# Optimization experiments

Measured on AMD Instinct MI355X. Metric: run time of the kernel, lower is better.

Reference implementation:

```python
import jax, jax.numpy as jnp
import numpy as np

N_EMBD = 4096
N_LAYERS = 32
LAYER = 3


def _layer_norm(x, w, b, eps=1e-5):
    mu = jnp.mean(x)
    var = jnp.var(x)
    return (x - mu) * jax.lax.rsqrt(var + eps) * w + b


def setup_inputs() -> dict:
    key = jax.random.key(0)
    ks = jax.random.split(key, 12)
    s = np.float32(1.0 / np.sqrt(N_EMBD))  # keep matvec outputs O(1) so exp() stays sane
    return {
        "input": jax.random.normal(ks[0], (N_EMBD,), jnp.float32),
        "state": jax.random.normal(ks[1], (5 * N_LAYERS, N_EMBD), jnp.float32) * 0.1,
        "time_mix_k": jax.random.uniform(ks[2], (N_EMBD,), jnp.float32),
        "time_mix_v": jax.random.uniform(ks[3], (N_EMBD,), jnp.float32),
        "time_mix_r": jax.random.uniform(ks[4], (N_EMBD,), jnp.float32),
        "time_first": jax.random.normal(ks[5], (N_EMBD,), jnp.float32) * 0.5,
        "time_decay": -jnp.abs(jax.random.normal(ks[6], (N_EMBD,), jnp.float32)),
        "kw": jax.random.normal(ks[7], (N_EMBD, N_EMBD), jnp.float32) * s,
        "vw": jax.random.normal(ks[8], (N_EMBD, N_EMBD), jnp.float32) * s,
        "rw": jax.random.normal(ks[9], (N_EMBD, N_EMBD), jnp.float32) * s,
        "ow": jax.random.normal(ks[10], (N_EMBD, N_EMBD), jnp.float32) * s,
        "ln_weight": jnp.ones((N_EMBD,), jnp.float32),
        "ln_bias": jnp.zeros((N_EMBD,), jnp.float32),
        "layer_num": LAYER,
        "n_embd": N_EMBD,
    }


def reference(input, state, time_mix_k, time_mix_v, time_mix_r, time_first,
              time_decay, kw, vw, rw, ow, ln_weight, ln_bias, layer_num, n_embd):
    # FLOAT_MODE == 'fp32' branch of the original module.
    i = int(layer_num)
    x = _layer_norm(input, ln_weight, ln_bias)

    prev = state[5 * i + 1]  # previous token's post-LN x (time shift)
    xk = x * time_mix_k + prev * (1.0 - time_mix_k)
    xv = x * time_mix_v + prev * (1.0 - time_mix_v)
    xr = x * time_mix_r + prev * (1.0 - time_mix_r)

    r = jax.nn.sigmoid(rw @ xr)
    kk = kw @ xk
    vv = vw @ xv

    aa = state[5 * i + 2]
    bb = state[5 * i + 3]
    pp = state[5 * i + 4]  # running log-max for numerical stability

    # WKV output for this token
    ww = time_first + kk
    p = jnp.maximum(pp, ww)
    e1 = jnp.exp(pp - p)
    e2 = jnp.exp(ww - p)
    a = e1 * aa + e2 * vv
    b = e1 * bb + e2

    # state update
    ww2 = pp + time_decay
    p2 = jnp.maximum(ww2, kk)
    e1s = jnp.exp(ww2 - p2)
    e2s = jnp.exp(kk - p2)
    new_aa = e1s * aa + e2s * vv
    new_bb = e1s * bb + e2s

    new_state = (state
                 .at[5 * i + 1].set(x)
                 .at[5 * i + 2].set(new_aa)
                 .at[5 * i + 3].set(new_bb)
                 .at[5 * i + 4].set(p2))

    wkv = a / b
    out = ow @ (r * wkv)
    return (new_state, out)
```

## Files before the change

### kernel.cpp

```cpp
#include <hip/hip_runtime.h>
#include <math.h>

#define NE 4096
#define NROWS_STATE 160

#define WS_XK   0
#define WS_XV   (NE)
#define WS_XR   (2*NE)
#define WS_KK   (3*NE)
#define WS_VV   (4*NE)
#define WS_RR   (5*NE)
#define WS_RWKV (6*NE)

__device__ __forceinline__ float wave_reduce_sum(float v) {
    #pragma unroll
    for (int off = 32; off > 0; off >>= 1)
        v += __shfl_down(v, off, 64);
    return v;
}

__global__ void __launch_bounds__(256)
k_copy_ln_mix(const float* __restrict__ in, const float* __restrict__ state,
              const float* __restrict__ tmk, const float* __restrict__ tmv,
              const float* __restrict__ tmr, const float* __restrict__ lnw,
              const float* __restrict__ lnb, const int* __restrict__ layer,
              float* __restrict__ out_state, float* __restrict__ out_vec,
              float* __restrict__ ws) {
    int li = layer[0];
    if (blockIdx.x >= 641) {
        int zidx = (blockIdx.x - 641) * 256 + threadIdx.x;
        float4 z = make_float4(0.f, 0.f, 0.f, 0.f);
        if (zidx < 3 * NE / 4) ((float4*)(ws + WS_KK))[zidx] = z;
        else                   ((float4*)out_vec)[zidx - 3 * NE / 4] = z;
        return;
    }
    if (blockIdx.x != 0) {
        int i4 = (blockIdx.x - 1) * 256 + threadIdx.x;
        int row = i4 >> 10;
        if (row < 5 * li + 1 || row > 5 * li + 4) {
            ((float4*)out_state)[i4] = ((const float4*)state)[i4];
        }
        return;
    }
    __shared__ float sm1[4];
    __shared__ float sm2[4];
    __shared__ float s_mu, s_rstd;
    int t = threadIdx.x;
    int lane = t & 63, wid = t >> 6;

    float4 v[4];
    float sum = 0.0f, sumsq = 0.0f;
    #pragma unroll
    for (int j = 0; j < 4; ++j) {
        v[j] = ((const float4*)in)[t * 4 + j];
        sum   += v[j].x + v[j].y + v[j].z + v[j].w;
        sumsq += v[j].x*v[j].x + v[j].y*v[j].y + v[j].z*v[j].z + v[j].w*v[j].w;
    }
    float s1 = wave_reduce_sum(sum);
    float s2 = wave_reduce_sum(sumsq);
    if (lane == 0) { sm1[wid] = s1; sm2[wid] = s2; }
    __syncthreads();
    if (t == 0) {
        float tot  = sm1[0] + sm1[1] + sm1[2] + sm1[3];
        float tot2 = sm2[0] + sm2[1] + sm2[2] + sm2[3];
        float mu  = tot * (1.0f / NE);
        float var = tot2 * (1.0f / NE) - mu * mu;
        s_mu = mu;
        s_rstd = rsqrtf(var + 1e-5f);
    }
    __syncthreads();
    float mu = s_mu, rstd = s_rstd;

    const float* prev_row = state + (size_t)(5 * li + 1) * NE;
    float* x_row = out_state + (size_t)(5 * li + 1) * NE;

    #pragma unroll
    for (int j = 0; j < 4; ++j) {
        #pragma unroll
        for (int c = 0; c < 4; ++c) {
            int idx = t * 16 + j * 4 + c;
            float xin = (c == 0) ? v[j].x : (c == 1) ? v[j].y : (c == 2) ? v[j].z : v[j].w;
            float x    = (xin - mu) * rstd * lnw[idx] + lnb[idx];
            float prev = prev_row[idx];
            float mk = tmk[idx], mv = tmv[idx], mr = tmr[idx];
            ws[WS_XK + idx] = x * mk + prev * (1.0f - mk);
            ws[WS_XV + idx] = x * mv + prev * (1.0f - mv);
            ws[WS_XR + idx] = x * mr + prev * (1.0f - mr);
            x_row[idx] = x;
        }
    }
}

__global__ void __launch_bounds__(256)
k_matvec3(const float* __restrict__ kw, const float* __restrict__ vw,
          const float* __restrict__ rw, const float* __restrict__ ws_in,
          float* __restrict__ ws_out) {
    int t    = threadIdx.x;
    int lane = t & 63;
    int g    = blockIdx.x * 4 + (t >> 6);
    int m    = g >> 14;
    int rem  = g & 16383;
    int row  = rem >> 2;
    int seg  = rem & 3;
    const float* W = (m == 0) ? kw : (m == 1) ? vw : rw;
    const float4* Wr = (const float4*)(W + (size_t)row * NE) + seg * 256;
    const float4* xv = (const float4*)(ws_in + m * NE) + seg * 256;

    float acc = 0.0f;
    #pragma unroll
    for (int i = 0; i < 4; ++i) {
        float4 w4 = Wr[i * 64 + lane];
        float4 x4 = xv[i * 64 + lane];
        acc += w4.x*x4.x + w4.y*x4.y + w4.z*x4.z + w4.w*x4.w;
    }
    acc = wave_reduce_sum(acc);
    if (lane == 0) atomicAdd(&ws_out[m * NE + row], acc);
}

__global__ void k_wkv(const float* __restrict__ state, const float* __restrict__ tf,
                      const float* __restrict__ td, const int* __restrict__ layer,
                      const float* __restrict__ ws, float* __restrict__ out_state,
                      float* __restrict__ rwkv) {
    int idx = blockIdx.x * blockDim.x + threadIdx.x;
    if (idx >= NE) return;
    int li = layer[0];
    float kk = ws[WS_KK + idx];
    float vv = ws[WS_VV + idx];
    float r  = 1.0f / (1.0f + expf(-ws[WS_RR + idx]));
    float aa = state[(size_t)(5 * li + 2) * NE + idx];
    float bb = state[(size_t)(5 * li + 3) * NE + idx];
    float pp = state[(size_t)(5 * li + 4) * NE + idx];

    float ww = tf[idx] + kk;
    float p  = fmaxf(pp, ww);
    float e1 = expf(pp - p);
    float e2 = expf(ww - p);
    float a  = e1 * aa + e2 * vv;
    float b  = e1 * bb + e2;

    float ww2 = pp + td[idx];
    float p2  = fmaxf(ww2, kk);
    float e1s = expf(ww2 - p2);
    float e2s = expf(kk - p2);
    out_state[(size_t)(5 * li + 2) * NE + idx] = e1s * aa + e2s * vv;
    out_state[(size_t)(5 * li + 3) * NE + idx] = e1s * bb + e2s;
    out_state[(size_t)(5 * li + 4) * NE + idx] = p2;

    rwkv[idx] = r * (a / b);
}

__global__ void __launch_bounds__(256)
k_matvec_ow(const float* __restrict__ ow, const float* __restrict__ rwkv,
            float* __restrict__ out) {
    int t    = threadIdx.x;
    int lane = t & 63;
    int g    = blockIdx.x * 4 + (t >> 6);
    int row  = g >> 2;
    int seg  = g & 3;
    const float4* Wr = (const float4*)(ow + (size_t)row * NE) + seg * 256;
    const float4* xv = (const float4*)rwkv + seg * 256;

    float acc = 0.0f;
    #pragma unroll
    for (int i = 0; i < 4; ++i) {
        float4 w4 = Wr[i * 64 + lane];
        float4 x4 = xv[i * 64 + lane];
        acc += w4.x*x4.x + w4.y*x4.y + w4.z*x4.z + w4.w*x4.w;
    }
    acc = wave_reduce_sum(acc);
    if (lane == 0) atomicAdd(&out[row], acc);
}

extern "C" void kernel_launch(void* const* d_in, const int* in_sizes, int n_in,
                              void* d_out, int out_size, void* d_ws, size_t ws_size,
                              hipStream_t stream) {
    const float* input = (const float*)d_in[0];
    const float* state = (const float*)d_in[1];
    const float* tmk   = (const float*)d_in[2];
    const float* tmv   = (const float*)d_in[3];
    const float* tmr   = (const float*)d_in[4];
    const float* tf    = (const float*)d_in[5];
    const float* td    = (const float*)d_in[6];
    const float* kw    = (const float*)d_in[7];
    const float* vw    = (const float*)d_in[8];
    const float* rw    = (const float*)d_in[9];
    const float* ow    = (const float*)d_in[10];
    const float* lnw   = (const float*)d_in[11];
    const float* lnb   = (const float*)d_in[12];
    const int*   layer = (const int*)d_in[13];

    float* out_state = (float*)d_out;
    float* out_vec   = (float*)d_out + (size_t)NROWS_STATE * NE;
    float* ws        = (float*)d_ws;

    k_copy_ln_mix<<<657, 256, 0, stream>>>(input, state, tmk, tmv, tmr, lnw, lnb,
                                           layer, out_state, out_vec, ws);
    k_matvec3<<<3 * NE, 256, 0, stream>>>(kw, vw, rw, ws, ws + WS_KK);
    k_wkv<<<NE / 256, 256, 0, stream>>>(state, tf, td, layer, ws, out_state,
                                        ws + WS_RWKV);
    k_matvec_ow<<<NE, 256, 0, stream>>>(ow, ws + WS_RWKV, out_vec);
}
```

Baseline: 56.48 us.

## Fuse layernorm and mixing into k/v/r matvec, drop atomics and zeroing

Every block of the k/v/r matvec kernel now recomputes the layernorm statistics and the token-mix vector into shared memory, which removes the separate mix kernel and its workspace round trip. Each wave computes a full row dot product, so the split-row atomicAdds and the zero-initialisation of outputs are no longer needed. The state copy moves into the wkv kernel, and the ow matvec stages its input vector in shared memory. The cost is redundant layernorm work in roughly three thousand blocks and 16 KB of shared memory per block, which may reduce occupancy.

```diff
diff --git a/kernel.cpp b/kernel.cpp
--- a/kernel.cpp
+++ b/kernel.cpp
@@ -4,13 +4,10 @@
 #define NE 4096
 #define NROWS_STATE 160
 
-#define WS_XK   0
-#define WS_XV   (NE)
-#define WS_XR   (2*NE)
-#define WS_KK   (3*NE)
-#define WS_VV   (4*NE)
-#define WS_RR   (5*NE)
-#define WS_RWKV (6*NE)
+#define WS_KK   0
+#define WS_VV   (NE)
+#define WS_RR   (2*NE)
+#define WS_RWKV (3*NE)
 
 __device__ __forceinline__ float wave_reduce_sum(float v) {
     #pragma unroll
@@ -20,33 +17,18 @@
 }
 
 __global__ void __launch_bounds__(256)
-k_copy_ln_mix(const float* __restrict__ in, const float* __restrict__ state,
-              const float* __restrict__ tmk, const float* __restrict__ tmv,
-              const float* __restrict__ tmr, const float* __restrict__ lnw,
-              const float* __restrict__ lnb, const int* __restrict__ layer,
-              float* __restrict__ out_state, float* __restrict__ out_vec,
-              float* __restrict__ ws) {
+k_ln_matvec3(const float* __restrict__ in, const float* __restrict__ state,
+             const float* __restrict__ tmk, const float* __restrict__ tmv,
+             const float* __restrict__ tmr, const float* __restrict__ lnw,
+             const float* __restrict__ lnb, const int* __restrict__ layer,
+             const float* __restrict__ kw, const float* __restrict__ vw,
+             const float* __restrict__ rw, float* __restrict__ out_state,
+             float* __restrict__ ws_out) {
+    __shared__ float4 sx[NE / 4];
+    __shared__ float sred[8];
+    __shared__ float s_stats[2];
+    int t = threadIdx.x, lane = t & 63, wid = t >> 6;
     int li = layer[0];
-    if (blockIdx.x >= 641) {
-        int zidx = (blockIdx.x - 641) * 256 + threadIdx.x;
-        float4 z = make_float4(0.f, 0.f, 0.f, 0.f);
-        if (zidx < 3 * NE / 4) ((float4*)(ws + WS_KK))[zidx] = z;
-        else                   ((float4*)out_vec)[zidx - 3 * NE / 4] = z;
-        return;
-    }
-    if (blockIdx.x != 0) {
-        int i4 = (blockIdx.x - 1) * 256 + threadIdx.x;
-        int row = i4 >> 10;
-        if (row < 5 * li + 1 || row > 5 * li + 4) {
-            ((float4*)out_state)[i4] = ((const float4*)state)[i4];
-        }
-        return;
-    }
-    __shared__ float sm1[4];
-    __shared__ float sm2[4];
-    __shared__ float s_mu, s_rstd;
-    int t = threadIdx.x;
-    int lane = t & 63, wid = t >> 6;
 
     float4 v[4];
     float sum = 0.0f, sumsq = 0.0f;
@@ -58,72 +40,77 @@
     }
     float s1 = wave_reduce_sum(sum);
     float s2 = wave_reduce_sum(sumsq);
-    if (lane == 0) { sm1[wid] = s1; sm2[wid] = s2; }
+    if (lane == 0) { sred[wid] = s1; sred[4 + wid] = s2; }
     __syncthreads();
     if (t == 0) {
-        float tot  = sm1[0] + sm1[1] + sm1[2] + sm1[3];
-        float tot2 = sm2[0] + sm2[1] + sm2[2] + sm2[3];
+        float tot  = sred[0] + sred[1] + sred[2] + sred[3];
+        float tot2 = sred[4] + sred[5] + sred[6] + sred[7];
         float mu  = tot * (1.0f / NE);
         float var = tot2 * (1.0f / NE) - mu * mu;
-        s_mu = mu;
-        s_rstd = rsqrtf(var + 1e-5f);
+        s_stats[0] = mu;
+        s_stats[1] = rsqrtf(var + 1e-5f);
     }
     __syncthreads();
-    float mu = s_mu, rstd = s_rstd;
+    float mu = s_stats[0], rstd = s_stats[1];
 
+    if (blockIdx.x >= 3072) {
+        int e = (blockIdx.x - 3072) * 256 + t;
+        float x = (in[e] - mu) * rstd * lnw[e] + lnb[e];
+        out_state[(size_t)(5 * li + 1) * NE + e] = x;
+        return;
+    }
+
+    int m    = blockIdx.x >> 10;
+    int rowg = blockIdx.x & 1023;
+    const float* tm = (m == 0) ? tmk : (m == 1) ? tmv : tmr;
     const float* prev_row = state + (size_t)(5 * li + 1) * NE;
-    float* x_row = out_state + (size_t)(5 * li + 1) * NE;
 
     #pragma unroll
     for (int j = 0; j < 4; ++j) {
-        #pragma unroll
-        for (int c = 0; c < 4; ++c) {
-            int idx = t * 16 + j * 4 + c;
-            float xin = (c == 0) ? v[j].x : (c == 1) ? v[j].y : (c == 2) ? v[j].z : v[j].w;
-            float x    = (xin - mu) * rstd * lnw[idx] + lnb[idx];
-            float prev = prev_row[idx];
-            float mk = tmk[idx], mv = tmv[idx], mr = tmr[idx];
-            ws[WS_XK + idx] = x * mk + prev * (1.0f - mk);
-            ws[WS_XV + idx] = x * mv + prev * (1.0f - mv);
-            ws[WS_XR + idx] = x * mr + prev * (1.0f - mr);
-            x_row[idx] = x;
-        }
+        int i4 = t * 4 + j;
+        float4 xin = v[j];
+        float4 tm4 = ((const float4*)tm)[i4];
+        float4 pv4 = ((const float4*)prev_row)[i4];
+        float4 lw4 = ((const float4*)lnw)[i4];
+        float4 lb4 = ((const float4*)lnb)[i4];
+        float4 r;
+        r.x = ((xin.x - mu) * rstd * lw4.x + lb4.x) * tm4.x + pv4.x * (1.0f - tm4.x);
+        r.y = ((xin.y - mu) * rstd * lw4.y + lb4.y) * tm4.y + pv4.y * (1.0f - tm4.y);
+        r.z = ((xin.z - mu) * rstd * lw4.z + lb4.z) * tm4.z + pv4.z * (1.0f - tm4.z);
+        r.w = ((xin.w - mu) * rstd * lw4.w + lb4.w) * tm4.w + pv4.w * (1.0f - tm4.w);
+        sx[i4] = r;
     }
+    __syncthreads();
+
+    int row = rowg * 4 + wid;
+    const float* W = (m == 0) ? kw : (m == 1) ? vw : rw;
+    const float4* Wr = (const float4*)(W + (size_t)row * NE);
+    float acc = 0.0f;
+    #pragma unroll
+    for (int i = 0; i < 16; ++i) {
+        float4 w4 = Wr[i * 64 + lane];
+        float4 x4 = sx[i * 64 + lane];
+        acc += w4.x*x4.x + w4.y*x4.y + w4.z*x4.z + w4.w*x4.w;
+    }
+    acc = wave_reduce_sum(acc);
+    if (lane == 0) ws_out[m * NE + row] = acc;
 }
 
 __global__ void __launch_bounds__(256)
-k_matvec3(const float* __restrict__ kw, const float* __restrict__ vw,
-          const float* __restrict__ rw, const float* __restrict__ ws_in,
-          float* __restrict__ ws_out) {
-    int t    = threadIdx.x;
-    int lane = t & 63;
-    int g    = blockIdx.x * 4 + (t >> 6);
-    int m    = g >> 14;
-    int rem  = g & 16383;
-    int row  = rem >> 2;
-    int seg  = rem & 3;
-    const float* W = (m == 0) ? kw : (m == 1) ? vw : rw;
-    const float4* Wr = (const float4*)(W + (size_t)row * NE) + seg * 256;
-    const float4* xv = (const float4*)(ws_in + m * NE) + seg * 256;
-
-    float acc = 0.0f;
-    #pragma unroll
-    for (int i = 0; i < 4; ++i) {
-        float4 w4 = Wr[i * 64 + lane];
-        float4 x4 = xv[i * 64 + lane];
-        acc += w4.x*x4.x + w4.y*x4.y + w4.z*x4.z + w4.w*x4.w;
+k_wkv_copy(const float* __restrict__ state, const float* __restrict__ tf,
+           const float* __restrict__ td, const int* __restrict__ layer,
+           const float* __restrict__ ws, float* __restrict__ out_state,
+           float* __restrict__ rwkv) {
+    int li = layer[0];
+    if (blockIdx.x >= 16) {
+        int i4 = (blockIdx.x - 16) * 256 + threadIdx.x;
+        int row = i4 >> 10;
+        if (row < 5 * li + 1 || row > 5 * li + 4) {
+            ((float4*)out_state)[i4] = ((const float4*)state)[i4];
+        }
+        return;
     }
-    acc = wave_reduce_sum(acc);
-    if (lane == 0) atomicAdd(&ws_out[m * NE + row], acc);
-}
-
-__global__ void k_wkv(const float* __restrict__ state, const float* __restrict__ tf,
-                      const float* __restrict__ td, const int* __restrict__ layer,
-                      const float* __restrict__ ws, float* __restrict__ out_state,
-                      float* __restrict__ rwkv) {
-    int idx = blockIdx.x * blockDim.x + threadIdx.x;
-    if (idx >= NE) return;
-    int li = layer[0];
+    int idx = blockIdx.x * 256 + threadIdx.x;
     float kk = ws[WS_KK + idx];
     float vv = ws[WS_VV + idx];
     float r  = 1.0f / (1.0f + expf(-ws[WS_RR + idx]));
@@ -152,23 +139,24 @@
 __global__ void __launch_bounds__(256)
 k_matvec_ow(const float* __restrict__ ow, const float* __restrict__ rwkv,
             float* __restrict__ out) {
+    __shared__ float4 sx[NE / 4];
     int t    = threadIdx.x;
     int lane = t & 63;
-    int g    = blockIdx.x * 4 + (t >> 6);
-    int row  = g >> 2;
-    int seg  = g & 3;
-    const float4* Wr = (const float4*)(ow + (size_t)row * NE) + seg * 256;
-    const float4* xv = (const float4*)rwkv + seg * 256;
+    int row  = blockIdx.x * 4 + (t >> 6);
+    #pragma unroll
+    for (int j = 0; j < 4; ++j) sx[t + j * 256] = ((const float4*)rwkv)[t + j * 256];
+    __syncthreads();
 
+    const float4* Wr = (const float4*)(ow + (size_t)row * NE);
     float acc = 0.0f;
     #pragma unroll
-    for (int i = 0; i < 4; ++i) {
+    for (int i = 0; i < 16; ++i) {
         float4 w4 = Wr[i * 64 + lane];
-        float4 x4 = xv[i * 64 + lane];
+        float4 x4 = sx[i * 64 + lane];
         acc += w4.x*x4.x + w4.y*x4.y + w4.z*x4.z + w4.w*x4.w;
     }
     acc = wave_reduce_sum(acc);
-    if (lane == 0) atomicAdd(&out[row], acc);
+    if (lane == 0) out[row] = acc;
 }
 
 extern "C" void kernel_launch(void* const* d_in, const int* in_sizes, int n_in,
@@ -193,10 +181,9 @@
     float* out_vec   = (float*)d_out + (size_t)NROWS_STATE * NE;
     float* ws        = (float*)d_ws;
 
-    k_copy_ln_mix<<<657, 256, 0, stream>>>(input, state, tmk, tmv, tmr, lnw, lnb,
-                                           layer, out_state, out_vec, ws);
-    k_matvec3<<<3 * NE, 256, 0, stream>>>(kw, vw, rw, ws, ws + WS_KK);
-    k_wkv<<<NE / 256, 256, 0, stream>>>(state, tf, td, layer, ws, out_state,
+    k_ln_matvec3<<<3088, 256, 0, stream>>>(input, state, tmk, tmv, tmr, lnw, lnb,
+                                           layer, kw, vw, rw, out_state, ws + WS_KK);
+    k_wkv_copy<<<656, 256, 0, stream>>>(state, tf, td, layer, ws, out_state,
                                         ws + WS_RWKV);
-    k_matvec_ow<<<NE, 256, 0, stream>>>(ow, ws + WS_RWKV, out_vec);
+    k_matvec_ow<<<NE / 4, 256, 0, stream>>>(ow, ws + WS_RWKV, out_vec);
 }
```

New measurement: 59.32 us. 5.0% more time.

## Fuse k/v/r matvecs with WKV and drop split-K atomics

Applied to the files above, without the earlier changes.

Each wave now computes a full row of all three k, v and r matvecs and then runs the WKV update directly for that row. This removes the separate WKV kernel, the zero-init blocks and the atomicAdds. The output matvec also uses one wave per full row with the input vector staged in shared memory, and writes results directly instead of accumulating atomically. The cost is fewer blocks (1024 instead of 12288) with longer per-wave loops, which lowers parallelism and could limit memory-level parallelism.

```diff
diff --git a/kernel.cpp b/kernel.cpp
--- a/kernel.cpp
+++ b/kernel.cpp
@@ -7,10 +7,7 @@
 #define WS_XK   0
 #define WS_XV   (NE)
 #define WS_XR   (2*NE)
-#define WS_KK   (3*NE)
-#define WS_VV   (4*NE)
-#define WS_RR   (5*NE)
-#define WS_RWKV (6*NE)
+#define WS_RWKV (3*NE)
 
 __device__ __forceinline__ float wave_reduce_sum(float v) {
     #pragma unroll
@@ -24,16 +21,8 @@
               const float* __restrict__ tmk, const float* __restrict__ tmv,
               const float* __restrict__ tmr, const float* __restrict__ lnw,
               const float* __restrict__ lnb, const int* __restrict__ layer,
-              float* __restrict__ out_state, float* __restrict__ out_vec,
-              float* __restrict__ ws) {
+              float* __restrict__ out_state, float* __restrict__ ws) {
     int li = layer[0];
-    if (blockIdx.x >= 641) {
-        int zidx = (blockIdx.x - 641) * 256 + threadIdx.x;
-        float4 z = make_float4(0.f, 0.f, 0.f, 0.f);
-        if (zidx < 3 * NE / 4) ((float4*)(ws + WS_KK))[zidx] = z;
-        else                   ((float4*)out_vec)[zidx - 3 * NE / 4] = z;
-        return;
-    }
     if (blockIdx.x != 0) {
         int i4 = (blockIdx.x - 1) * 256 + threadIdx.x;
         int row = i4 >> 10;
@@ -92,83 +81,84 @@
 }
 
 __global__ void __launch_bounds__(256)
-k_matvec3(const float* __restrict__ kw, const float* __restrict__ vw,
-          const float* __restrict__ rw, const float* __restrict__ ws_in,
-          float* __restrict__ ws_out) {
+k_matvec3_wkv(const float* __restrict__ kw, const float* __restrict__ vw,
+              const float* __restrict__ rw, const float* __restrict__ ws,
+              const float* __restrict__ state, const float* __restrict__ tf,
+              const float* __restrict__ td, const int* __restrict__ layer,
+              float* __restrict__ out_state, float* __restrict__ rwkv) {
     int t    = threadIdx.x;
     int lane = t & 63;
-    int g    = blockIdx.x * 4 + (t >> 6);
-    int m    = g >> 14;
-    int rem  = g & 16383;
-    int row  = rem >> 2;
-    int seg  = rem & 3;
-    const float* W = (m == 0) ? kw : (m == 1) ? vw : rw;
-    const float4* Wr = (const float4*)(W + (size_t)row * NE) + seg * 256;
-    const float4* xv = (const float4*)(ws_in + m * NE) + seg * 256;
+    int row  = blockIdx.x * 4 + (t >> 6);
 
-    float acc = 0.0f;
+    const float4* Wk = (const float4*)(kw + (size_t)row * NE);
+    const float4* Wv = (const float4*)(vw + (size_t)row * NE);
+    const float4* Wr = (const float4*)(rw + (size_t)row * NE);
+    const float4* xk = (const float4*)(ws + WS_XK);
+    const float4* xv = (const float4*)(ws + WS_XV);
+    const float4* xr = (const float4*)(ws + WS_XR);
+
+    float ak = 0.0f, av = 0.0f, ar = 0.0f;
     #pragma unroll
-    for (int i = 0; i < 4; ++i) {
-        float4 w4 = Wr[i * 64 + lane];
-        float4 x4 = xv[i * 64 + lane];
-        acc += w4.x*x4.x + w4.y*x4.y + w4.z*x4.z + w4.w*x4.w;
+    for (int i = 0; i < 16; ++i) {
+        float4 w_, x_;
+        w_ = Wk[i * 64 + lane]; x_ = xk[i * 64 + lane];
+        ak += w_.x*x_.x + w_.y*x_.y + w_.z*x_.z + w_.w*x_.w;
+        w_ = Wv[i * 64 + lane]; x_ = xv[i * 64 + lane];
+        av += w_.x*x_.x + w_.y*x_.y + w_.z*x_.z + w_.w*x_.w;
+        w_ = Wr[i * 64 + lane]; x_ = xr[i * 64 + lane];
+        ar += w_.x*x_.x + w_.y*x_.y + w_.z*x_.z + w_.w*x_.w;
     }
-    acc = wave_reduce_sum(acc);
-    if (lane == 0) atomicAdd(&ws_out[m * NE + row], acc);
-}
+    float kk = wave_reduce_sum(ak);
+    float vv = wave_reduce_sum(av);
+    float rr = wave_reduce_sum(ar);
 
-__global__ void k_wkv(const float* __restrict__ state, const float* __restrict__ tf,
-                      const float* __restrict__ td, const int* __restrict__ layer,
-                      const float* __restrict__ ws, float* __restrict__ out_state,
-                      float* __restrict__ rwkv) {
-    int idx = blockIdx.x * blockDim.x + threadIdx.x;
-    if (idx >= NE) return;
-    int li = layer[0];
-    float kk = ws[WS_KK + idx];
-    float vv = ws[WS_VV + idx];
-    float r  = 1.0f / (1.0f + expf(-ws[WS_RR + idx]));
-    float aa = state[(size_t)(5 * li + 2) * NE + idx];
-    float bb = state[(size_t)(5 * li + 3) * NE + idx];
-    float pp = state[(size_t)(5 * li + 4) * NE + idx];
+    if (lane == 0) {
+        int li = layer[0];
+        float r  = 1.0f / (1.0f + expf(-rr));
+        float aa = state[(size_t)(5 * li + 2) * NE + row];
+        float bb = state[(size_t)(5 * li + 3) * NE + row];
+        float pp = state[(size_t)(5 * li + 4) * NE + row];
 
-    float ww = tf[idx] + kk;
-    float p  = fmaxf(pp, ww);
-    float e1 = expf(pp - p);
-    float e2 = expf(ww - p);
-    float a  = e1 * aa + e2 * vv;
-    float b  = e1 * bb + e2;
+        float ww = tf[row] + kk;
+        float p  = fmaxf(pp, ww);
+        float e1 = expf(pp - p);
+        float e2 = expf(ww - p);
+        float a  = e1 * aa + e2 * vv;
+        float b  = e1 * bb + e2;
 
-    float ww2 = pp + td[idx];
-    float p2  = fmaxf(ww2, kk);
-    float e1s = expf(ww2 - p2);
-    float e2s = expf(kk - p2);
-    out_state[(size_t)(5 * li + 2) * NE + idx] = e1s * aa + e2s * vv;
-    out_state[(size_t)(5 * li + 3) * NE + idx] = e1s * bb + e2s;
-    out_state[(size_t)(5 * li + 4) * NE + idx] = p2;
+        float ww2 = pp + td[row];
+        float p2  = fmaxf(ww2, kk);
+        float e1s = expf(ww2 - p2);
+        float e2s = expf(kk - p2);
+        out_state[(size_t)(5 * li + 2) * NE + row] = e1s * aa + e2s * vv;
+        out_state[(size_t)(5 * li + 3) * NE + row] = e1s * bb + e2s;
+        out_state[(size_t)(5 * li + 4) * NE + row] = p2;
 
-    rwkv[idx] = r * (a / b);
+        rwkv[row] = r * (a / b);
+    }
 }
 
 __global__ void __launch_bounds__(256)
 k_matvec_ow(const float* __restrict__ ow, const float* __restrict__ rwkv,
             float* __restrict__ out) {
+    __shared__ float4 sx[NE / 4];
     int t    = threadIdx.x;
     int lane = t & 63;
-    int g    = blockIdx.x * 4 + (t >> 6);
-    int row  = g >> 2;
-    int seg  = g & 3;
-    const float4* Wr = (const float4*)(ow + (size_t)row * NE) + seg * 256;
-    const float4* xv = (const float4*)rwkv + seg * 256;
+    int row  = blockIdx.x * 4 + (t >> 6);
+    #pragma unroll
+    for (int j = 0; j < 4; ++j) sx[t + j * 256] = ((const float4*)rwkv)[t + j * 256];
+    __syncthreads();
 
+    const float4* Wr = (const float4*)(ow + (size_t)row * NE);
     float acc = 0.0f;
     #pragma unroll
-    for (int i = 0; i < 4; ++i) {
+    for (int i = 0; i < 16; ++i) {
         float4 w4 = Wr[i * 64 + lane];
-        float4 x4 = xv[i * 64 + lane];
+        float4 x4 = sx[i * 64 + lane];
         acc += w4.x*x4.x + w4.y*x4.y + w4.z*x4.z + w4.w*x4.w;
     }
     acc = wave_reduce_sum(acc);
-    if (lane == 0) atomicAdd(&out[row], acc);
+    if (lane == 0) out[row] = acc;
 }
 
 extern "C" void kernel_launch(void* const* d_in, const int* in_sizes, int n_in,
@@ -193,10 +183,9 @@
     float* out_vec   = (float*)d_out + (size_t)NROWS_STATE * NE;
     float* ws        = (float*)d_ws;
 
-    k_copy_ln_mix<<<657, 256, 0, stream>>>(input, state, tmk, tmv, tmr, lnw, lnb,
-                                           layer, out_state, out_vec, ws);
-    k_matvec3<<<3 * NE, 256, 0, stream>>>(kw, vw, rw, ws, ws + WS_KK);
-    k_wkv<<<NE / 256, 256, 0, stream>>>(state, tf, td, layer, ws, out_state,
-                                        ws + WS_RWKV);
-    k_matvec_ow<<<NE, 256, 0, stream>>>(ow, ws + WS_RWKV, out_vec);
+    k_copy_ln_mix<<<641, 256, 0, stream>>>(input, state, tmk, tmv, tmr, lnw, lnb,
+                                           layer, out_state, ws);
+    k_matvec3_wkv<<<NE / 4, 256, 0, stream>>>(kw, vw, rw, ws, state, tf, td,
+                                              layer, out_state, ws + WS_RWKV);
+    k_matvec_ow<<<NE / 4, 256, 0, stream>>>(ow, ws + WS_RWKV, out_vec);
 }
```

Result: slower. 58.74 us (+4.0%).
